# Kernel optimization log

Hardware: AMD Instinct MI355X
Metric: run time of the kernel (lower is better)

## Reference

```python
import jax, jax.numpy as jnp
import numpy as np

N = 100000; K = 16; D = 3; CIN = 64; CD = 16; CT = CIN + CD; DM = 2; COUT = 128; EPS = 1e-5

@jax.custom_vjp
def ste_sign(x):
    return jnp.sign(x)

def _ste_fwd(x):
    return jnp.sign(x), x

def _ste_bwd(x, g):
    return (g * (jnp.abs(x) <= 1.0).astype(g.dtype),)

ste_sign.defvjp(_ste_fwd, _ste_bwd)

def hardtanh(x):
    return jnp.clip(x, -1.0, 1.0)

def bn(x, g, b, m, v):
    # eval-mode BatchNorm1d over the last (channel) axis
    return (x - m) * jax.lax.rsqrt(v + EPS) * g + b

def bilinear(x, w, b):
    # binarized linear: sign(activation) @ sign(weight)^T + bias
    return ste_sign(x) @ ste_sign(w).T + b

def bigconv(x, w, b):
    # grouped binarized Conv1d with groups == in_channels and kernel_size == length,
    # so output length is 1. x: (N, C, K), w: (C*m, K) -> (N, C*m)
    C = x.shape[1]
    m = w.shape[0] // C
    wb = ste_sign(w).reshape(C, m, w.shape[1])
    return jnp.einsum('nck,cjk->ncj', ste_sign(x), wb).reshape(x.shape[0], -1) + b

def setup_inputs() -> dict:
    key = jax.random.key(0)
    ks = iter(jax.random.split(key, 64))
    def rn(shape, s=0.1):
        return jax.random.normal(next(ks), shape, dtype=jnp.float32) * s
    inp = {}
    inp['x'] = jax.random.normal(next(ks), (N, CIN), dtype=jnp.float32)
    inp['pos'] = jax.random.normal(next(ks), (N, D), dtype=jnp.float32)
    inp['col'] = jax.random.randint(next(ks), (N, K), 0, N, dtype=jnp.int32)
    def bn_params(c, pre):
        inp[pre + 'g'] = 1.0 + rn((c,))
        inp[pre + 'b'] = rn((c,))
        inp[pre + 'm'] = rn((c,))
        inp[pre + 'v'] = jax.random.uniform(next(ks), (c,), dtype=jnp.float32) + 0.5
    inp['W1'] = rn((CD, D), 0.5); inp['b1'] = rn((CD,)); bn_params(CD, 'bn1')
    inp['W2'] = rn((CD, CD), 0.5); inp['b2'] = rn((CD,)); bn_params(CD, 'bn2')
    inp['Wm'] = rn((K * K, D * K), 0.5); inp['bm'] = rn((K * K,)); bn_params(K * K, 'bn3')
    inp['cw1'] = rn((K * K, K), 0.5); inp['cb1'] = rn((K * K,)); bn_params(K * K, 'bn4')
    inp['cw2'] = rn((K * K, K), 0.5); inp['cb2'] = rn((K * K,)); bn_params(K * K, 'bn5')
    inp['cw3'] = rn((CT * DM, K), 0.5); inp['cb3'] = rn((CT * DM,))
    inp['Wf'] = rn((COUT, CT * DM), 0.5); inp['bf'] = rn((COUT,))
    return inp

def reference(x, pos, col,
              W1, b1, bn1g, bn1b, bn1m, bn1v,
              W2, b2, bn2g, bn2b, bn2m, bn2v,
              Wm, bm, bn3g, bn3b, bn3m, bn3v,
              cw1, cb1, bn4g, bn4b, bn4m, bn4v,
              cw2, cb2, bn5g, bn5b, bn5m, bn5v,
              cw3, cb3, Wf, bf):
    # relative neighbor positions: (N, K, D)
    pd = pos[col] - pos[:, None, :]
    # mlp1: per gathered point feature lift dim -> C_delta (first layer is plain Lin, ifFirst=True)
    h = bn(hardtanh(pd.reshape(N * K, D) @ W1.T + b1), bn1g, bn1b, bn1m, bn1v)
    h = bn(hardtanh(bilinear(h, W2, b2)), bn2g, bn2b, bn2m, bn2v)
    # concat lifted features with gathered input features: (N, CT, K)
    xs = jnp.concatenate([h.reshape(N, K, CD), x[col]], axis=-1).transpose(0, 2, 1)
    # mlp2: per-point KxK transform matrix
    t = bn(hardtanh(pd.reshape(N, K * D) @ Wm.T + bm), bn3g, bn3b, bn3m, bn3v)
    t = bn(hardtanh(bigconv(t.reshape(N, K, K), cw1, cb1)), bn4g, bn4b, bn4m, bn4v)
    T = bn(bigconv(t.reshape(N, K, K), cw2, cb2), bn5g, bn5b, bn5m, bn5v).reshape(N, K, K)
    # per-point batched matmul: (N,1,K,K) @ (N,CT,K,1) -> (N,CT,K)
    xt = jnp.einsum('nij,ncj->nci', T, xs)
    # final grouped binarized conv (length K -> 1) + binarized linear
    out = bilinear(bigconv(xt, cw3, cb3), Wf, bf)
    return out
```

## Files before the change

### kernel.cpp

```cpp
#include <hip/hip_runtime.h>

#define NPTS 100000
#define KN 16
#define DIM 3
#define CIN 64
#define CD 16
#define CT 80
#define COUT 128
#define PTS 4
#define EPSV 1e-5f

__device__ __align__(16) float g_wmt[48 * 256];
__device__ __align__(16) float g_w2f[256];
__device__ __align__(16) float g_cw1f[4096];
__device__ __align__(16) float g_cw2f[4096];
__device__ unsigned g_cw3[2][160];
__device__ uint2    g_wf2[10 * 128];

__device__ __forceinline__ float sgnf(float x) {
    return (x > 0.f) ? 1.f : ((x < 0.f) ? -1.f : 0.f);
}
__device__ __forceinline__ float clamp1(float x) { return fminf(1.f, fmaxf(-1.f, x)); }
__device__ __forceinline__ unsigned rot16(unsigned w) { return (w >> 16) | (w << 16); }

__device__ __forceinline__ unsigned packrow16(const float* __restrict__ w) {
    unsigned pos = 0, neg = 0;
    #pragma unroll
    for (int k = 0; k < 16; ++k) {
        pos |= (w[k] > 0.f ? 1u : 0u) << k;
        neg |= (w[k] < 0.f ? 1u : 0u) << k;
    }
    return (neg << 16) | pos;
}

__device__ __forceinline__ int tdot(unsigned a, unsigned wp, unsigned wr) {
    return __popc(a & wp) - __popc(a & wr);
}

__global__ void prep_kernel(const float* __restrict__ Wm, const float* __restrict__ W2,
                            const float* __restrict__ cw1, const float* __restrict__ cw2,
                            const float* __restrict__ cw3, const float* __restrict__ Wf) {
    int b = blockIdx.x, t = threadIdx.x;
    if (b < 48) {
        int ib = b >> 2, ii = b & 3;
        g_wmt[(ib * 256 + t) * 4 + ii] = Wm[t * 48 + b];
    } else if (b == 48) {
        #pragma unroll
        for (int k = 0; k < 16; ++k) g_cw1f[t * 16 + k] = sgnf(cw1[t * 16 + k]);
    } else if (b == 49) {
        #pragma unroll
        for (int k = 0; k < 16; ++k) g_cw2f[t * 16 + k] = sgnf(cw2[t * 16 + k]);
    } else if (b == 50) {
        if (t < 160) { unsigned w = packrow16(cw3 + t * 16); g_cw3[0][t] = w; g_cw3[1][t] = rot16(w); }
        else if (t < 176) {
            int c = t - 160;
            #pragma unroll
            for (int j = 0; j < 16; ++j) g_w2f[c * 16 + j] = sgnf(W2[c * 16 + j]);
        }
    } else {
        if (t < 128) {
            for (int m = 0; m < 10; ++m) {
                unsigned w = packrow16(Wf + t * 160 + m * 16);
                g_wf2[m * 128 + t] = make_uint2(w, rot16(w));
            }
        }
    }
}

__global__ __launch_bounds__(256) void bixconv_kernel(
    const float* __restrict__ x, const float* __restrict__ pos, const int* __restrict__ col,
    const float* __restrict__ W1, const float* __restrict__ b1,
    const float* __restrict__ bn1g, const float* __restrict__ bn1b, const float* __restrict__ bn1m, const float* __restrict__ bn1v,
    const float* __restrict__ b2,
    const float* __restrict__ bn2g, const float* __restrict__ bn2b, const float* __restrict__ bn2m, const float* __restrict__ bn2v,
    const float* __restrict__ bm,
    const float* __restrict__ bn3g, const float* __restrict__ bn3b, const float* __restrict__ bn3m, const float* __restrict__ bn3v,
    const float* __restrict__ cb1,
    const float* __restrict__ bn4g, const float* __restrict__ bn4b, const float* __restrict__ bn4m, const float* __restrict__ bn4v,
    const float* __restrict__ cb2,
    const float* __restrict__ bn5g, const float* __restrict__ bn5b, const float* __restrict__ bn5m, const float* __restrict__ bn5v,
    const float* __restrict__ cb3, const float* __restrict__ bf,
    float* __restrict__ out)
{
    __shared__ int sIdx[PTS][KN];
    __shared__ __align__(16) float sPd[PTS][48];
    __shared__ __align__(16) float sXs[PTS][CT][20];
    __shared__ __align__(16) float sT[PTS][KN][20];
    __shared__ __align__(16) float sSgnH[PTS][KN][16];
    __shared__ __align__(16) float sSgn1[PTS][256];
    __shared__ __align__(16) float sSgn2[PTS][256];
    __shared__ unsigned sPkXt[PTS][CT];
    __shared__ unsigned sPkY[PTS][10];

    const int tid = threadIdx.x;
    const int lane = tid & 63;
    const int nb = blockIdx.x * PTS;

    if (tid < PTS * KN) {
        int p = tid >> 4, k = tid & 15;
        int n = nb + p;
        int idx = col[n * KN + k];
        sIdx[p][k] = idx;
        float ax = pos[n * 3 + 0], ay = pos[n * 3 + 1], az = pos[n * 3 + 2];
        sPd[p][k * 3 + 0] = pos[idx * 3 + 0] - ax;
        sPd[p][k * 3 + 1] = pos[idx * 3 + 1] - ay;
        sPd[p][k * 3 + 2] = pos[idx * 3 + 2] - az;
    }
    __syncthreads();

    {
        int p = tid >> 6, c = lane;
        #pragma unroll
        for (int kb = 0; kb < 4; ++kb) {
            float4 v;
            v.x = x[(size_t)sIdx[p][kb * 4 + 0] * CIN + c];
            v.y = x[(size_t)sIdx[p][kb * 4 + 1] * CIN + c];
            v.z = x[(size_t)sIdx[p][kb * 4 + 2] * CIN + c];
            v.w = x[(size_t)sIdx[p][kb * 4 + 3] * CIN + c];
            *(float4*)&sXs[p][CD + c][kb * 4] = v;
        }
    }
    {
        int c = tid & 15, k = tid >> 4;
        float w0 = W1[c * 3 + 0], w1 = W1[c * 3 + 1], w2v = W1[c * 3 + 2];
        float bb = b1[c];
        float s = bn1g[c] * rsqrtf(bn1v[c] + EPSV);
        float tt = bn1b[c] - bn1m[c] * s;
        #pragma unroll
        for (int p = 0; p < PTS; ++p) {
            float z = sPd[p][k * 3 + 0] * w0 + sPd[p][k * 3 + 1] * w1 + sPd[p][k * 3 + 2] * w2v + bb;
            float v = clamp1(z) * s + tt;
            sSgnH[p][k][c] = sgnf(v);
        }
    }
    __syncthreads();

    {
        int c = tid & 15, k = tid >> 4;
        float4 w0 = *(const float4*)&g_w2f[c * 16 + 0];
        float4 w1 = *(const float4*)&g_w2f[c * 16 + 4];
        float4 w2 = *(const float4*)&g_w2f[c * 16 + 8];
        float4 w3 = *(const float4*)&g_w2f[c * 16 + 12];
        float bb = b2[c];
        float s = bn2g[c] * rsqrtf(bn2v[c] + EPSV);
        float tt = bn2b[c] - bn2m[c] * s;
        #pragma unroll
        for (int p = 0; p < PTS; ++p) {
            float4 a0 = *(const float4*)&sSgnH[p][k][0];
            float4 a1 = *(const float4*)&sSgnH[p][k][4];
            float4 a2 = *(const float4*)&sSgnH[p][k][8];
            float4 a3 = *(const float4*)&sSgnH[p][k][12];
            float acc = bb;
            acc += a0.x * w0.x; acc += a0.y * w0.y; acc += a0.z * w0.z; acc += a0.w * w0.w;
            acc += a1.x * w1.x; acc += a1.y * w1.y; acc += a1.z * w1.z; acc += a1.w * w1.w;
            acc += a2.x * w2.x; acc += a2.y * w2.y; acc += a2.z * w2.z; acc += a2.w * w2.w;
            acc += a3.x * w3.x; acc += a3.y * w3.y; acc += a3.z * w3.z; acc += a3.w * w3.w;
            sXs[p][c][k] = clamp1(acc) * s + tt;
        }
    }
    {
        int j = tid;
        float acc0 = 0.f, acc1 = 0.f, acc2 = 0.f, acc3 = 0.f;
        #pragma unroll 2
        for (int ib = 0; ib < 12; ++ib) {
            float4 w  = *(const float4*)&g_wmt[(ib * 256 + j) * 4];
            float4 q0 = *(const float4*)&sPd[0][ib * 4];
            float4 q1 = *(const float4*)&sPd[1][ib * 4];
            float4 q2 = *(const float4*)&sPd[2][ib * 4];
            float4 q3 = *(const float4*)&sPd[3][ib * 4];
            acc0 += w.x * q0.x; acc1 += w.x * q1.x; acc2 += w.x * q2.x; acc3 += w.x * q3.x;
            acc0 += w.y * q0.y; acc1 += w.y * q1.y; acc2 += w.y * q2.y; acc3 += w.y * q3.y;
            acc0 += w.z * q0.z; acc1 += w.z * q1.z; acc2 += w.z * q2.z; acc3 += w.z * q3.z;
            acc0 += w.w * q0.w; acc1 += w.w * q1.w; acc2 += w.w * q2.w; acc3 += w.w * q3.w;
        }
        float bb = bm[j];
        float s = bn3g[j] * rsqrtf(bn3v[j] + EPSV);
        float tt = bn3b[j] - bn3m[j] * s;
        float vv[PTS] = {acc0, acc1, acc2, acc3};
        #pragma unroll
        for (int p = 0; p < PTS; ++p) {
            float v = clamp1(vv[p] + bb) * s + tt;
            sSgn1[p][j] = sgnf(v);
        }
    }
    __syncthreads();

    {
        int r = tid, c = r >> 4;
        float4 w0 = *(const float4*)&g_cw1f[r * 16 + 0];
        float4 w1 = *(const float4*)&g_cw1f[r * 16 + 4];
        float4 w2 = *(const float4*)&g_cw1f[r * 16 + 8];
        float4 w3 = *(const float4*)&g_cw1f[r * 16 + 12];
        float bb = cb1[r];
        float s = bn4g[r] * rsqrtf(bn4v[r] + EPSV);
        float tt = bn4b[r] - bn4m[r] * s;
        #pragma unroll
        for (int p = 0; p < PTS; ++p) {
            float4 a0 = *(const float4*)&sSgn1[p][c * 16 + 0];
            float4 a1 = *(const float4*)&sSgn1[p][c * 16 + 4];
            float4 a2 = *(const float4*)&sSgn1[p][c * 16 + 8];
            float4 a3 = *(const float4*)&sSgn1[p][c * 16 + 12];
            float acc = bb;
            acc += a0.x * w0.x; acc += a0.y * w0.y; acc += a0.z * w0.z; acc += a0.w * w0.w;
            acc += a1.x * w1.x; acc += a1.y * w1.y; acc += a1.z * w1.z; acc += a1.w * w1.w;
            acc += a2.x * w2.x; acc += a2.y * w2.y; acc += a2.z * w2.z; acc += a2.w * w2.w;
            acc += a3.x * w3.x; acc += a3.y * w3.y; acc += a3.z * w3.z; acc += a3.w * w3.w;
            float v = clamp1(acc) * s + tt;
            sSgn2[p][r] = sgnf(v);
        }
    }
    __syncthreads();

    {
        int r = tid, c = r >> 4;
        float4 w0 = *(const float4*)&g_cw2f[r * 16 + 0];
        float4 w1 = *(const float4*)&g_cw2f[r * 16 + 4];
        float4 w2 = *(const float4*)&g_cw2f[r * 16 + 8];
        float4 w3 = *(const float4*)&g_cw2f[r * 16 + 12];
        float bb = cb2[r];
        float s = bn5g[r] * rsqrtf(bn5v[r] + EPSV);
        float tt = bn5b[r] - bn5m[r] * s;
        int i = r >> 4, jj = r & 15;
        #pragma unroll
        for (int p = 0; p < PTS; ++p) {
            float4 a0 = *(const float4*)&sSgn2[p][c * 16 + 0];
            float4 a1 = *(const float4*)&sSgn2[p][c * 16 + 4];
            float4 a2 = *(const float4*)&sSgn2[p][c * 16 + 8];
            float4 a3 = *(const float4*)&sSgn2[p][c * 16 + 12];
            float acc = bb;
            acc += a0.x * w0.x; acc += a0.y * w0.y; acc += a0.z * w0.z; acc += a0.w * w0.w;
            acc += a1.x * w1.x; acc += a1.y * w1.y; acc += a1.z * w1.z; acc += a1.w * w1.w;
            acc += a2.x * w2.x; acc += a2.y * w2.y; acc += a2.z * w2.z; acc += a2.w * w2.w;
            acc += a3.x * w3.x; acc += a3.y * w3.y; acc += a3.z * w3.z; acc += a3.w * w3.w;
            sT[p][i][jj] = acc * s + tt;
        }
    }
    __syncthreads();

    {
        int p = tid >> 6;
        int i = lane & 15, cg = lane >> 4;
        float4 t0 = *(const float4*)&sT[p][i][0];
        float4 t1 = *(const float4*)&sT[p][i][4];
        float4 t2 = *(const float4*)&sT[p][i][8];
        float4 t3 = *(const float4*)&sT[p][i][12];
        #pragma unroll 2
        for (int it = 0; it < 20; ++it) {
            int c = 4 * it + cg;
            float4 r0 = *(const float4*)&sXs[p][c][0];
            float4 r1 = *(const float4*)&sXs[p][c][4];
            float4 r2 = *(const float4*)&sXs[p][c][8];
            float4 r3 = *(const float4*)&sXs[p][c][12];
            float acc = 0.f;
            acc += t0.x * r0.x; acc += t0.y * r0.y; acc += t0.z * r0.z; acc += t0.w * r0.w;
            acc += t1.x * r1.x; acc += t1.y * r1.y; acc += t1.z * r1.z; acc += t1.w * r1.w;
            acc += t2.x * r2.x; acc += t2.y * r2.y; acc += t2.z * r2.z; acc += t2.w * r2.w;
            acc += t3.x * r3.x; acc += t3.y * r3.y; acc += t3.z * r3.z; acc += t3.w * r3.w;
            unsigned long long bp = __ballot(acc > 0.f);
            unsigned long long bn_ = __ballot(acc < 0.f);
            if ((lane & 15) == 0) {
                unsigned sh = lane & 48;
                sPkXt[p][c] = ((unsigned)((bn_ >> sh) & 0xFFFFull) << 16) |
                               (unsigned)((bp >> sh) & 0xFFFFull);
            }
        }
    }
    __syncthreads();

    if (tid < CT * 2) {
        int q = tid, c = q >> 1;
        unsigned wp = g_cw3[0][q], wr = g_cw3[1][q];
        float bb = cb3[q];
        #pragma unroll
        for (int p = 0; p < PTS; ++p) {
            unsigned a = sPkXt[p][c];
            float v = (float)tdot(a, wp, wr) + bb;
            unsigned long long bp = __ballot(v > 0.f);
            unsigned long long bn_ = __ballot(v < 0.f);
            if ((lane & 15) == 0) {
                unsigned sh = lane & 48;
                sPkY[p][q >> 4] = ((unsigned)((bn_ >> sh) & 0xFFFFull) << 16) |
                                   (unsigned)((bp >> sh) & 0xFFFFull);
            }
        }
    }
    __syncthreads();

    {
        int o = tid & 127, pp = tid >> 7;
        float bb = bf[o];
        unsigned a0[10], a1[10];
        #pragma unroll
        for (int m = 0; m < 10; ++m) { a0[m] = sPkY[2 * pp][m]; a1[m] = sPkY[2 * pp + 1][m]; }
        int acc0 = 0, acc1 = 0;
        #pragma unroll
        for (int m = 0; m < 10; ++m) {
            uint2 w = g_wf2[m * 128 + o];
            acc0 += __popc(a0[m] & w.x) - __popc(a0[m] & w.y);
            acc1 += __popc(a1[m] & w.x) - __popc(a1[m] & w.y);
        }
        out[(size_t)(nb + 2 * pp + 0) * COUT + o] = (float)acc0 + bb;
        out[(size_t)(nb + 2 * pp + 1) * COUT + o] = (float)acc1 + bb;
    }
}

extern "C" void kernel_launch(void* const* d_in, const int* in_sizes, int n_in,
                              void* d_out, int out_size, void* d_ws, size_t ws_size,
                              hipStream_t stream) {
    const float* x    = (const float*)d_in[0];
    const float* pos  = (const float*)d_in[1];
    const int*   col  = (const int*)d_in[2];
    const float* W1   = (const float*)d_in[3];
    const float* b1   = (const float*)d_in[4];
    const float* bn1g = (const float*)d_in[5];
    const float* bn1b = (const float*)d_in[6];
    const float* bn1m = (const float*)d_in[7];
    const float* bn1v = (const float*)d_in[8];
    const float* W2   = (const float*)d_in[9];
    const float* b2   = (const float*)d_in[10];
    const float* bn2g = (const float*)d_in[11];
    const float* bn2b = (const float*)d_in[12];
    const float* bn2m = (const float*)d_in[13];
    const float* bn2v = (const float*)d_in[14];
    const float* Wm   = (const float*)d_in[15];
    const float* bm   = (const float*)d_in[16];
    const float* bn3g = (const float*)d_in[17];
    const float* bn3b = (const float*)d_in[18];
    const float* bn3m = (const float*)d_in[19];
    const float* bn3v = (const float*)d_in[20];
    const float* cw1  = (const float*)d_in[21];
    const float* cb1  = (const float*)d_in[22];
    const float* bn4g = (const float*)d_in[23];
    const float* bn4b = (const float*)d_in[24];
    const float* bn4m = (const float*)d_in[25];
    const float* bn4v = (const float*)d_in[26];
    const float* cw2  = (const float*)d_in[27];
    const float* cb2  = (const float*)d_in[28];
    const float* bn5g = (const float*)d_in[29];
    const float* bn5b = (const float*)d_in[30];
    const float* bn5m = (const float*)d_in[31];
    const float* bn5v = (const float*)d_in[32];
    const float* cw3  = (const float*)d_in[33];
    const float* cb3  = (const float*)d_in[34];
    const float* Wf   = (const float*)d_in[35];
    const float* bf   = (const float*)d_in[36];
    float* outp = (float*)d_out;

    hipLaunchKernelGGL(prep_kernel, dim3(52), dim3(256), 0, stream, Wm, W2, cw1, cw2, cw3, Wf);
    hipLaunchKernelGGL(bixconv_kernel, dim3(NPTS / PTS), dim3(256), 0, stream,
        x, pos, col,
        W1, b1, bn1g, bn1b, bn1m, bn1v,
        b2, bn2g, bn2b, bn2m, bn2v,
        bm, bn3g, bn3b, bn3m, bn3v,
        cb1, bn4g, bn4b, bn4m, bn4v,
        cb2, bn5g, bn5b, bn5m, bn5v,
        cb3, bf, outp);
}
```

Before: 328.7 us.

## Interleave per-point activations and use packed FP32 FMA for small matmuls

Shared activation buffers are relaid so the four points of a block sit next to each other for each feature. Weights are stored duplicated in global memory, so that v_pk_fma_f32 can process two points per instruction in the mlp1, mlp2 and bigconv stages. Shared buffers are also aliased and reused, which shrinks the LDS footprint. In exchange, weight memory traffic doubles and inline asm may constrain the compiler's scheduling.

```diff
diff --git a/kernel.cpp b/kernel.cpp
--- a/kernel.cpp
+++ b/kernel.cpp
@@ -10,10 +10,19 @@
 #define PTS 4
 #define EPSV 1e-5f
 
-__device__ __align__(16) float g_wmt[48 * 256];
-__device__ __align__(16) float g_w2f[256];
-__device__ __align__(16) float g_cw1f[4096];
-__device__ __align__(16) float g_cw2f[4096];
+typedef float v2f __attribute__((ext_vector_type(2)));
+
+__device__ __forceinline__ v2f pkfma(v2f a, v2f b, v2f c) {
+    asm("v_pk_fma_f32 %0, %1, %2, %0" : "+v"(c) : "v"(a), "v"(b));
+    return c;
+}
+__device__ __forceinline__ v2f lo2(float4 v) { v2f r; r.x = v.x; r.y = v.y; return r; }
+__device__ __forceinline__ v2f hi2(float4 v) { v2f r; r.x = v.z; r.y = v.w; return r; }
+
+__device__ __align__(16) float g_wmt2[12 * 256 * 8];
+__device__ __align__(16) float g_w2f2[512];
+__device__ __align__(16) float g_cw1f2[8192];
+__device__ __align__(16) float g_cw2f2[8192];
 __device__ unsigned g_cw3[2][160];
 __device__ uint2    g_wf2[10 * 128];
 
@@ -43,19 +52,33 @@
     int b = blockIdx.x, t = threadIdx.x;
     if (b < 48) {
         int ib = b >> 2, ii = b & 3;
-        g_wmt[(ib * 256 + t) * 4 + ii] = Wm[t * 48 + b];
+        float w = Wm[t * 48 + b];
+        g_wmt2[(ib * 256 + t) * 8 + ii * 2 + 0] = w;
+        g_wmt2[(ib * 256 + t) * 8 + ii * 2 + 1] = w;
     } else if (b == 48) {
         #pragma unroll
-        for (int k = 0; k < 16; ++k) g_cw1f[t * 16 + k] = sgnf(cw1[t * 16 + k]);
+        for (int k = 0; k < 16; ++k) {
+            float w = sgnf(cw1[t * 16 + k]);
+            g_cw1f2[t * 32 + k * 2 + 0] = w;
+            g_cw1f2[t * 32 + k * 2 + 1] = w;
+        }
     } else if (b == 49) {
         #pragma unroll
-        for (int k = 0; k < 16; ++k) g_cw2f[t * 16 + k] = sgnf(cw2[t * 16 + k]);
+        for (int k = 0; k < 16; ++k) {
+            float w = sgnf(cw2[t * 16 + k]);
+            g_cw2f2[t * 32 + k * 2 + 0] = w;
+            g_cw2f2[t * 32 + k * 2 + 1] = w;
+        }
     } else if (b == 50) {
         if (t < 160) { unsigned w = packrow16(cw3 + t * 16); g_cw3[0][t] = w; g_cw3[1][t] = rot16(w); }
         else if (t < 176) {
             int c = t - 160;
             #pragma unroll
-            for (int j = 0; j < 16; ++j) g_w2f[c * 16 + j] = sgnf(W2[c * 16 + j]);
+            for (int j = 0; j < 16; ++j) {
+                float w = sgnf(W2[c * 16 + j]);
+                g_w2f2[c * 32 + j * 2 + 0] = w;
+                g_w2f2[c * 32 + j * 2 + 1] = w;
+            }
         }
     } else {
         if (t < 128) {
@@ -83,14 +106,16 @@
     float* __restrict__ out)
 {
     __shared__ int sIdx[PTS][KN];
-    __shared__ __align__(16) float sPd[PTS][48];
+    __shared__ __align__(16) float sPdI[48 * 4];
     __shared__ __align__(16) float sXs[PTS][CT][20];
     __shared__ __align__(16) float sT[PTS][KN][20];
-    __shared__ __align__(16) float sSgnH[PTS][KN][16];
-    __shared__ __align__(16) float sSgn1[PTS][256];
-    __shared__ __align__(16) float sSgn2[PTS][256];
-    __shared__ unsigned sPkXt[PTS][CT];
-    __shared__ unsigned sPkY[PTS][10];
+    __shared__ __align__(16) float sSgnHIbuf[256 * 4];
+    __shared__ __align__(16) float sSgn1I[256 * 4];
+
+    float* sSgnHI = sSgnHIbuf;
+    float* sSgn2I = sSgnHIbuf;
+    unsigned (*sPkXt)[CT] = reinterpret_cast<unsigned(*)[CT]>(&sSgn1I[0]);
+    unsigned (*sPkY)[10]  = reinterpret_cast<unsigned(*)[10]>(&sPdI[0]);
 
     const int tid = threadIdx.x;
     const int lane = tid & 63;
@@ -102,9 +127,9 @@
         int idx = col[n * KN + k];
         sIdx[p][k] = idx;
         float ax = pos[n * 3 + 0], ay = pos[n * 3 + 1], az = pos[n * 3 + 2];
-        sPd[p][k * 3 + 0] = pos[idx * 3 + 0] - ax;
-        sPd[p][k * 3 + 1] = pos[idx * 3 + 1] - ay;
-        sPd[p][k * 3 + 2] = pos[idx * 3 + 2] - az;
+        sPdI[(k * 3 + 0) * 4 + p] = pos[idx * 3 + 0] - ax;
+        sPdI[(k * 3 + 1) * 4 + p] = pos[idx * 3 + 1] - ay;
+        sPdI[(k * 3 + 2) * 4 + p] = pos[idx * 3 + 2] - az;
     }
     __syncthreads();
 
@@ -128,112 +153,116 @@
         float tt = bn1b[c] - bn1m[c] * s;
         #pragma unroll
         for (int p = 0; p < PTS; ++p) {
-            float z = sPd[p][k * 3 + 0] * w0 + sPd[p][k * 3 + 1] * w1 + sPd[p][k * 3 + 2] * w2v + bb;
+            float z = sPdI[(k * 3 + 0) * 4 + p] * w0 + sPdI[(k * 3 + 1) * 4 + p] * w1
+                    + sPdI[(k * 3 + 2) * 4 + p] * w2v + bb;
             float v = clamp1(z) * s + tt;
-            sSgnH[p][k][c] = sgnf(v);
+            sSgnHI[(k * 16 + c) * 4 + p] = sgnf(v);
         }
     }
     __syncthreads();
 
     {
         int c = tid & 15, k = tid >> 4;
-        float4 w0 = *(const float4*)&g_w2f[c * 16 + 0];
-        float4 w1 = *(const float4*)&g_w2f[c * 16 + 4];
-        float4 w2 = *(const float4*)&g_w2f[c * 16 + 8];
-        float4 w3 = *(const float4*)&g_w2f[c * 16 + 12];
+        const float4* wq = (const float4*)&g_w2f2[c * 32];
         float bb = b2[c];
         float s = bn2g[c] * rsqrtf(bn2v[c] + EPSV);
         float tt = bn2b[c] - bn2m[c] * s;
-        #pragma unroll
-        for (int p = 0; p < PTS; ++p) {
-            float4 a0 = *(const float4*)&sSgnH[p][k][0];
-            float4 a1 = *(const float4*)&sSgnH[p][k][4];
-            float4 a2 = *(const float4*)&sSgnH[p][k][8];
-            float4 a3 = *(const float4*)&sSgnH[p][k][12];
-            float acc = bb;
-            acc += a0.x * w0.x; acc += a0.y * w0.y; acc += a0.z * w0.z; acc += a0.w * w0.w;
-            acc += a1.x * w1.x; acc += a1.y * w1.y; acc += a1.z * w1.z; acc += a1.w * w1.w;
-            acc += a2.x * w2.x; acc += a2.y * w2.y; acc += a2.z * w2.z; acc += a2.w * w2.w;
-            acc += a3.x * w3.x; acc += a3.y * w3.y; acc += a3.z * w3.z; acc += a3.w * w3.w;
-            sXs[p][c][k] = clamp1(acc) * s + tt;
-        }
+        v2f acc01; acc01.x = bb; acc01.y = bb;
+        v2f acc23 = acc01;
+        #pragma unroll
+        for (int jj = 0; jj < 16; jj += 2) {
+            float4 wp = wq[jj >> 1];
+            float4 aA = *(const float4*)&sSgnHI[(k * 16 + jj) * 4];
+            float4 aB = *(const float4*)&sSgnHI[(k * 16 + jj + 1) * 4];
+            acc01 = pkfma(lo2(wp), lo2(aA), acc01);
+            acc23 = pkfma(lo2(wp), hi2(aA), acc23);
+            acc01 = pkfma(hi2(wp), lo2(aB), acc01);
+            acc23 = pkfma(hi2(wp), hi2(aB), acc23);
+        }
+        sXs[0][c][k] = clamp1(acc01.x) * s + tt;
+        sXs[1][c][k] = clamp1(acc01.y) * s + tt;
+        sXs[2][c][k] = clamp1(acc23.x) * s + tt;
+        sXs[3][c][k] = clamp1(acc23.y) * s + tt;
     }
     {
         int j = tid;
-        float acc0 = 0.f, acc1 = 0.f, acc2 = 0.f, acc3 = 0.f;
+        v2f acc01; acc01.x = 0.f; acc01.y = 0.f;
+        v2f acc23 = acc01;
         #pragma unroll 2
         for (int ib = 0; ib < 12; ++ib) {
-            float4 w  = *(const float4*)&g_wmt[(ib * 256 + j) * 4];
-            float4 q0 = *(const float4*)&sPd[0][ib * 4];
-            float4 q1 = *(const float4*)&sPd[1][ib * 4];
-            float4 q2 = *(const float4*)&sPd[2][ib * 4];
-            float4 q3 = *(const float4*)&sPd[3][ib * 4];
-            acc0 += w.x * q0.x; acc1 += w.x * q1.x; acc2 += w.x * q2.x; acc3 += w.x * q3.x;
-            acc0 += w.y * q0.y; acc1 += w.y * q1.y; acc2 += w.y * q2.y; acc3 += w.y * q3.y;
-            acc0 += w.z * q0.z; acc1 += w.z * q1.z; acc2 += w.z * q2.z; acc3 += w.z * q3.z;
-            acc0 += w.w * q0.w; acc1 += w.w * q1.w; acc2 += w.w * q2.w; acc3 += w.w * q3.w;
+            const float4* wq = (const float4*)&g_wmt2[(ib * 256 + j) * 8];
+            float4 wA = wq[0], wB = wq[1];
+            float4 q0 = *(const float4*)&sPdI[(ib * 4 + 0) * 4];
+            float4 q1 = *(const float4*)&sPdI[(ib * 4 + 1) * 4];
+            float4 q2 = *(const float4*)&sPdI[(ib * 4 + 2) * 4];
+            float4 q3 = *(const float4*)&sPdI[(ib * 4 + 3) * 4];
+            acc01 = pkfma(lo2(wA), lo2(q0), acc01); acc23 = pkfma(lo2(wA), hi2(q0), acc23);
+            acc01 = pkfma(hi2(wA), lo2(q1), acc01); acc23 = pkfma(hi2(wA), hi2(q1), acc23);
+            acc01 = pkfma(lo2(wB), lo2(q2), acc01); acc23 = pkfma(lo2(wB), hi2(q2), acc23);
+            acc01 = pkfma(hi2(wB), lo2(q3), acc01); acc23 = pkfma(hi2(wB), hi2(q3), acc23);
         }
         float bb = bm[j];
         float s = bn3g[j] * rsqrtf(bn3v[j] + EPSV);
         float tt = bn3b[j] - bn3m[j] * s;
-        float vv[PTS] = {acc0, acc1, acc2, acc3};
-        #pragma unroll
-        for (int p = 0; p < PTS; ++p) {
-            float v = clamp1(vv[p] + bb) * s + tt;
-            sSgn1[p][j] = sgnf(v);
-        }
+        float4 sg;
+        sg.x = sgnf(clamp1(acc01.x + bb) * s + tt);
+        sg.y = sgnf(clamp1(acc01.y + bb) * s + tt);
+        sg.z = sgnf(clamp1(acc23.x + bb) * s + tt);
+        sg.w = sgnf(clamp1(acc23.y + bb) * s + tt);
+        *(float4*)&sSgn1I[j * 4] = sg;
     }
     __syncthreads();
 
     {
         int r = tid, c = r >> 4;
-        float4 w0 = *(const float4*)&g_cw1f[r * 16 + 0];
-        float4 w1 = *(const float4*)&g_cw1f[r * 16 + 4];
-        float4 w2 = *(const float4*)&g_cw1f[r * 16 + 8];
-        float4 w3 = *(const float4*)&g_cw1f[r * 16 + 12];
+        const float4* wq = (const float4*)&g_cw1f2[r * 32];
         float bb = cb1[r];
         float s = bn4g[r] * rsqrtf(bn4v[r] + EPSV);
         float tt = bn4b[r] - bn4m[r] * s;
-        #pragma unroll
-        for (int p = 0; p < PTS; ++p) {
-            float4 a0 = *(const float4*)&sSgn1[p][c * 16 + 0];
-            float4 a1 = *(const float4*)&sSgn1[p][c * 16 + 4];
-            float4 a2 = *(const float4*)&sSgn1[p][c * 16 + 8];
-            float4 a3 = *(const float4*)&sSgn1[p][c * 16 + 12];
-            float acc = bb;
-            acc += a0.x * w0.x; acc += a0.y * w0.y; acc += a0.z * w0.z; acc += a0.w * w0.w;
-            acc += a1.x * w1.x; acc += a1.y * w1.y; acc += a1.z * w1.z; acc += a1.w * w1.w;
-            acc += a2.x * w2.x; acc += a2.y * w2.y; acc += a2.z * w2.z; acc += a2.w * w2.w;
-            acc += a3.x * w3.x; acc += a3.y * w3.y; acc += a3.z * w3.z; acc += a3.w * w3.w;
-            float v = clamp1(acc) * s + tt;
-            sSgn2[p][r] = sgnf(v);
-        }
+        v2f acc01; acc01.x = bb; acc01.y = bb;
+        v2f acc23 = acc01;
+        #pragma unroll
+        for (int kk = 0; kk < 16; kk += 2) {
+            float4 wp = wq[kk >> 1];
+            float4 aA = *(const float4*)&sSgn1I[(c * 16 + kk) * 4];
+            float4 aB = *(const float4*)&sSgn1I[(c * 16 + kk + 1) * 4];
+            acc01 = pkfma(lo2(wp), lo2(aA), acc01);
+            acc23 = pkfma(lo2(wp), hi2(aA), acc23);
+            acc01 = pkfma(hi2(wp), lo2(aB), acc01);
+            acc23 = pkfma(hi2(wp), hi2(aB), acc23);
+        }
+        float4 sg;
+        sg.x = sgnf(clamp1(acc01.x) * s + tt);
+        sg.y = sgnf(clamp1(acc01.y) * s + tt);
+        sg.z = sgnf(clamp1(acc23.x) * s + tt);
+        sg.w = sgnf(clamp1(acc23.y) * s + tt);
+        *(float4*)&sSgn2I[r * 4] = sg;
     }
     __syncthreads();
 
     {
         int r = tid, c = r >> 4;
-        float4 w0 = *(const float4*)&g_cw2f[r * 16 + 0];
-        float4 w1 = *(const float4*)&g_cw2f[r * 16 + 4];
-        float4 w2 = *(const float4*)&g_cw2f[r * 16 + 8];
-        float4 w3 = *(const float4*)&g_cw2f[r * 16 + 12];
+        const float4* wq = (const float4*)&g_cw2f2[r * 32];
         float bb = cb2[r];
         float s = bn5g[r] * rsqrtf(bn5v[r] + EPSV);
         float tt = bn5b[r] - bn5m[r] * s;
         int i = r >> 4, jj = r & 15;
-        #pragma unroll
-        for (int p = 0; p < PTS; ++p) {
-            float4 a0 = *(const float4*)&sSgn2[p][c * 16 + 0];
-            float4 a1 = *(const float4*)&sSgn2[p][c * 16 + 4];
-            float4 a2 = *(const float4*)&sSgn2[p][c * 16 + 8];
-            float4 a3 = *(const float4*)&sSgn2[p][c * 16 + 12];
-            float acc = bb;
-            acc += a0.x * w0.x; acc += a0.y * w0.y; acc += a0.z * w0.z; acc += a0.w * w0.w;
-            acc += a1.x * w1.x; acc += a1.y * w1.y; acc += a1.z * w1.z; acc += a1.w * w1.w;
-            acc += a2.x * w2.x; acc += a2.y * w2.y; acc += a2.z * w2.z; acc += a2.w * w2.w;
-            acc += a3.x * w3.x; acc += a3.y * w3.y; acc += a3.z * w3.z; acc += a3.w * w3.w;
-            sT[p][i][jj] = acc * s + tt;
-        }
+        v2f acc01; acc01.x = bb; acc01.y = bb;
+        v2f acc23 = acc01;
+        #pragma unroll
+        for (int kk = 0; kk < 16; kk += 2) {
+            float4 wp = wq[kk >> 1];
+            float4 aA = *(const float4*)&sSgn2I[(c * 16 + kk) * 4];
+            float4 aB = *(const float4*)&sSgn2I[(c * 16 + kk + 1) * 4];
+            acc01 = pkfma(lo2(wp), lo2(aA), acc01);
+            acc23 = pkfma(lo2(wp), hi2(aA), acc23);
+            acc01 = pkfma(hi2(wp), lo2(aB), acc01);
+            acc23 = pkfma(hi2(wp), hi2(aB), acc23);
+        }
+        sT[0][i][jj] = acc01.x * s + tt;
+        sT[1][i][jj] = acc01.y * s + tt;
+        sT[2][i][jj] = acc23.x * s + tt;
+        sT[3][i][jj] = acc23.y * s + tt;
     }
     __syncthreads();
 
```

Measured after the change: 475.3 us. 1.45x slower.
